# Kernel tuning notes

Measured on AMD Instinct MI355X. Metric: run time of the kernel, lower is better.

## Reference

```python
import jax, jax.numpy as jnp
import numpy as np

WS = 7      # window size
SHIFT = 3   # shift size
NH = 6      # num heads


def _window_partition(x, ws):
    # (b, h, w, c) -> (b * nh_w * nw_w, ws*ws, c)
    b, h, w, c = x.shape
    x = x.reshape(b, h // ws, ws, w // ws, ws, c).transpose(0, 1, 3, 2, 4, 5)
    return x.reshape(-1, ws * ws, c)


def _window_reverse(windows, h, w, ws):
    # (b*nw, ws, ws, c) -> (b, h, w, c)
    b = windows.shape[0] // ((h // ws) * (w // ws))
    x = windows.reshape(b, h // ws, w // ws, ws, ws, -1).transpose(0, 1, 3, 2, 4, 5)
    return x.reshape(b, h, w, -1)


def _rel_pos_index(ws):
    # WindowMSA._double_step_seq + flip, computed statically with numpy
    seq1 = np.arange(ws) * (2 * ws - 1)
    seq2 = np.arange(ws)
    coords = (seq1[:, None] + seq2[None, :]).reshape(-1)  # (ws*ws,)
    rel = coords[:, None] + coords[None, :]
    return np.ascontiguousarray(rel[:, ::-1])  # flip along dim 1


def _shift_mask(h_pad, w_pad, ws, shift):
    # Swin shifted-window attention mask, static numpy computation
    img = np.zeros((h_pad, w_pad), dtype=np.float32)
    slices = (slice(0, -ws), slice(-ws, -shift), slice(-shift, None))
    cnt = 0
    for hs in slices:
        for wsl in slices:
            img[hs, wsl] = cnt
            cnt += 1
    mw = img.reshape(h_pad // ws, ws, w_pad // ws, ws).transpose(0, 2, 1, 3)
    mw = mw.reshape(-1, ws * ws)  # (nw, n)
    diff = mw[:, None, :] - mw[:, :, None]
    return np.where(diff != 0, -100.0, 0.0).astype(np.float32)  # (nw, n, n)


def setup_inputs() -> dict:
    key = jax.random.key(0)
    ks = jax.random.split(key, 5)
    c, b, h, w = 192, 32, 56, 56
    return {
        "query": jax.random.normal(ks[0], (b, h * w, c), jnp.float32),
        "rpb_table": jax.random.normal(ks[1], ((2 * WS - 1) ** 2, NH), jnp.float32) * 0.02,
        "qkv_w": jax.random.normal(ks[2], (3 * c, c), jnp.float32) * 0.02,
        "qkv_b": jnp.zeros((3 * c,), jnp.float32),
        "proj_w": jax.random.normal(ks[3], (c, c), jnp.float32) * 0.02,
        "proj_b": jnp.zeros((c,), jnp.float32),
        "h": h,
        "w": w,
    }


def reference(query, rpb_table, qkv_w, qkv_b, proj_w, proj_b, h, w):
    b, l, c = query.shape
    hd = c // NH
    scale = hd ** (-0.5)
    x = query.reshape(b, h, w, c)
    pad_r = (WS - w % WS) % WS
    pad_b = (WS - h % WS) % WS
    if pad_r > 0 or pad_b > 0:
        x = jnp.pad(x, ((0, 0), (0, pad_b), (0, pad_r), (0, 0)))
    h_pad, w_pad = h + pad_b, w + pad_r

    # cyclic shift + mask
    x = jnp.roll(x, shift=(-SHIFT, -SHIFT), axis=(1, 2))
    attn_mask = jnp.asarray(_shift_mask(h_pad, w_pad, WS, SHIFT))  # (nw, n, n)

    xw = _window_partition(x, WS)  # (b*nw, n, c)
    B_, n, _ = xw.shape
    nw = attn_mask.shape[0]

    # qkv projection
    qkv = (xw @ qkv_w.T + qkv_b).reshape(B_, n, 3, NH, hd).transpose(2, 0, 3, 1, 4)
    q, k, v = qkv[0], qkv[1], qkv[2]  # each (B_, NH, n, hd)

    attn = jnp.einsum('bhqd,bhkd->bhqk', q * scale, k)

    # relative position bias
    rel_idx = jnp.asarray(_rel_pos_index(WS).reshape(-1))
    bias = rpb_table[rel_idx].reshape(n, n, NH).transpose(2, 0, 1)  # (NH, n, n)
    attn = attn + bias[None]

    # shifted-window mask
    attn = attn.reshape(B_ // nw, nw, NH, n, n) + attn_mask[None, :, None]
    attn = attn.reshape(B_, NH, n, n)

    attn = jax.nn.softmax(attn, axis=-1)
    out = jnp.einsum('bhqk,bhkd->bhqd', attn, v).transpose(0, 2, 1, 3).reshape(B_, n, c)
    out = out @ proj_w.T + proj_b

    out = out.reshape(-1, WS, WS, c)
    xr = _window_reverse(out, h_pad, w_pad, WS)
    xr = jnp.roll(xr, shift=(SHIFT, SHIFT), axis=(1, 2))
    if pad_r > 0 or pad_b > 0:
        xr = xr[:, :h, :w, :]
    return xr.reshape(b, h * w, c)
```

## Files before the change

kernel.cpp:

```cpp
#include <hip/hip_runtime.h>

typedef unsigned short u16;
typedef unsigned int   u32;
typedef __bf16 bf16x8 __attribute__((ext_vector_type(8)));
typedef float  f32x4  __attribute__((ext_vector_type(4)));


__device__ __forceinline__ u16 f2b(float f){
  return __builtin_bit_cast(u16, (__bf16)f);
}
__device__ __forceinline__ u32 pk2(float a, float b){
  return (u32)f2b(a) | ((u32)f2b(b) << 16);
}

__device__ __forceinline__ int coords_fn(int t){ return (t/7)*13 + (t%7); }
__device__ __forceinline__ int code_fn(int t, int wy, int wx){
  const int ty = t/7, tx = t%7;
  const int hp = wy*7 + ty, wp = wx*7 + tx;
  const int rh = (hp < 49) ? 0 : ((hp < 53) ? 1 : 2);
  const int rw = (wp < 49) ? 0 : ((wp < 53) ? 1 : 2);
  return rh*3 + rw;
}

__global__ __launch_bounds__(256) void prep_kernel(const float* __restrict__ qkvw,
                                                   const float* __restrict__ projw,
                                                   const float* __restrict__ rpb,
                                                   u16* __restrict__ wq, u16* __restrict__ wp,
                                                   float* __restrict__ biasC){
  const int i = blockIdx.x * 256 + threadIdx.x;
  if (i < 576*192) wq[i] = f2b(qkvw[i]);
  if (i < 192*192) wp[i] = f2b(projw[i]);
  {
    const int cls = i / 27648, rem = i % 27648;
    const int h = rem / 4608, rem2 = rem % 4608;
    const int ii = rem2 / 72, j = rem2 % 72;
    const int wyR = (cls & 2) ? 7 : 0, wxR = (cls & 1) ? 7 : 0;
    float v = -1e30f;
    if (j < 49){
      const int icl = (ii > 48) ? 48 : ii;
      v = rpb[(coords_fn(icl) + coords_fn(48 - j))*6 + h];
      if (code_fn(icl, wyR, wxR) != code_fn(j, wyR, wxR)) v -= 100.0f;
    }
    biasC[i] = v;
  }
}

__global__ __launch_bounds__(256, 2) void qkv_kernel(const float* __restrict__ x,
    const u16* __restrict__ wq, const float* __restrict__ qb,
    u16* __restrict__ qG, u16* __restrict__ kG, u16* __restrict__ vG)
{
  __shared__ u16 XA[128][200];
  const int wi0 = blockIdx.x * 2;
  const int bb = wi0 >> 6, wy = (wi0 >> 3) & 7;
  const int tid = threadIdx.x;
  const int wave = tid >> 6, lane = tid & 63;
  const int g = lane >> 4, r = lane & 15;
  const f32x4 z4 = {0.f, 0.f, 0.f, 0.f};

  #pragma unroll
  for (int half = 0; half < 2; ++half){
    float4 gv[6][2];
    int grow[6], gc8[6];
    #pragma unroll
    for (int i2 = 0; i2 < 6; ++i2){
      const int idx = half*1536 + i2*256 + tid;
      const int row = idx / 24, c8 = (idx % 24) * 8;
      grow[i2] = row; gc8[i2] = c8;
      const int rl = row & 63;
      const int wx = (wi0 + (row >> 6)) & 7;
      if (rl < 49){
        const int ty = rl / 7, tx = rl % 7;
        int sh = wy*7 + ty + 3; if (sh >= 56) sh -= 56;
        int sw = wx*7 + tx + 3; if (sw >= 56) sw -= 56;
        const float* src = x + (size_t)(((bb*56 + sh)*56 + sw))*192 + c8;
        gv[i2][0] = *reinterpret_cast<const float4*>(src);
        gv[i2][1] = *reinterpret_cast<const float4*>(src + 4);
      } else {
        gv[i2][0] = make_float4(0.f,0.f,0.f,0.f);
        gv[i2][1] = make_float4(0.f,0.f,0.f,0.f);
      }
    }
    #pragma unroll
    for (int i2 = 0; i2 < 6; ++i2){
      uint4 w;
      w.x = pk2(gv[i2][0].x, gv[i2][0].y);
      w.y = pk2(gv[i2][0].z, gv[i2][0].w);
      w.z = pk2(gv[i2][1].x, gv[i2][1].y);
      w.w = pk2(gv[i2][1].z, gv[i2][1].w);
      *reinterpret_cast<uint4*>(&XA[grow[i2]][gc8[i2]]) = w;
    }
  }
  __syncthreads();

  {
    f32x4 acc[8][3];
    #pragma unroll
    for (int mt = 0; mt < 8; ++mt)
      #pragma unroll
      for (int c = 0; c < 3; ++c) acc[mt][c] = z4;
    #pragma unroll
    for (int ks = 0; ks < 6; ++ks){
      bf16x8 aw[3];
      #pragma unroll
      for (int c = 0; c < 3; ++c)
        aw[c] = *reinterpret_cast<const bf16x8*>(wq + (size_t)(wave*48 + c*16 + r)*192 + ks*32 + 8*g);
      bf16x8 ax[8];
      #pragma unroll
      for (int mt = 0; mt < 8; ++mt)
        ax[mt] = *reinterpret_cast<const bf16x8*>(&XA[mt*16 + r][ks*32 + 8*g]);
      #pragma unroll
      for (int mt = 0; mt < 8; ++mt)
        #pragma unroll
        for (int c = 0; c < 3; ++c)
          acc[mt][c] = __builtin_amdgcn_mfma_f32_16x16x32_bf16(aw[c], ax[mt], acc[mt][c], 0, 0, 0);
    }
    const float S = 0.17677669529663687f;
    #pragma unroll
    for (int c = 0; c < 3; ++c){
      const int ch0 = wave*48 + c*16 + 4*g;
      const float4 bi = *reinterpret_cast<const float4*>(qb + ch0);
      #pragma unroll
      for (int mt = 0; mt < 8; ++mt){
        const int u = (wi0 + (mt >> 2))*6 + (ch0 >> 5);
        const int tok = (mt & 3)*16 + r;
        uint2 t;
        t.x = pk2((acc[mt][c][0] + bi.x)*S, (acc[mt][c][1] + bi.y)*S);
        t.y = pk2((acc[mt][c][2] + bi.z)*S, (acc[mt][c][3] + bi.w)*S);
        *reinterpret_cast<uint2*>(qG + ((size_t)u*64 + tok)*32 + (ch0 & 31)) = t;
      }
    }
  }

  {
    f32x4 acc[8][3];
    #pragma unroll
    for (int mt = 0; mt < 8; ++mt)
      #pragma unroll
      for (int c = 0; c < 3; ++c) acc[mt][c] = z4;
    #pragma unroll
    for (int ks = 0; ks < 6; ++ks){
      bf16x8 aw[3];
      #pragma unroll
      for (int c = 0; c < 3; ++c)
        aw[c] = *reinterpret_cast<const bf16x8*>(wq + (size_t)(192 + wave*48 + c*16 + r)*192 + ks*32 + 8*g);
      bf16x8 ax[8];
      #pragma unroll
      for (int mt = 0; mt < 8; ++mt)
        ax[mt] = *reinterpret_cast<const bf16x8*>(&XA[mt*16 + r][ks*32 + 8*g]);
      #pragma unroll
      for (int mt = 0; mt < 8; ++mt)
        #pragma unroll
        for (int c = 0; c < 3; ++c)
          acc[mt][c] = __builtin_amdgcn_mfma_f32_16x16x32_bf16(aw[c], ax[mt], acc[mt][c], 0, 0, 0);
    }
    #pragma unroll
    for (int c = 0; c < 3; ++c){
      const int ch0 = wave*48 + c*16 + 4*g;
      const float4 bi = *reinterpret_cast<const float4*>(qb + 192 + ch0);
      #pragma unroll
      for (int mt = 0; mt < 8; ++mt){
        const int u = (wi0 + (mt >> 2))*6 + (ch0 >> 5);
        const int tok = (mt & 3)*16 + r;
        uint2 t;
        t.x = pk2(acc[mt][c][0] + bi.x, acc[mt][c][1] + bi.y);
        t.y = pk2(acc[mt][c][2] + bi.z, acc[mt][c][3] + bi.w);
        *reinterpret_cast<uint2*>(kG + ((size_t)u*64 + tok)*32 + (ch0 & 31)) = t;
      }
    }
  }

  {
    f32x4 acc[8][3];
    #pragma unroll
    for (int mt = 0; mt < 8; ++mt)
      #pragma unroll
      for (int c = 0; c < 3; ++c) acc[mt][c] = z4;
    #pragma unroll
    for (int ks = 0; ks < 6; ++ks){
      bf16x8 bw[3];
      #pragma unroll
      for (int c = 0; c < 3; ++c)
        bw[c] = *reinterpret_cast<const bf16x8*>(wq + (size_t)(384 + wave*48 + c*16 + r)*192 + ks*32 + 8*g);
      bf16x8 ax[8];
      #pragma unroll
      for (int mt = 0; mt < 8; ++mt)
        ax[mt] = *reinterpret_cast<const bf16x8*>(&XA[mt*16 + r][ks*32 + 8*g]);
      #pragma unroll
      for (int mt = 0; mt < 8; ++mt)
        #pragma unroll
        for (int c = 0; c < 3; ++c)
          acc[mt][c] = __builtin_amdgcn_mfma_f32_16x16x32_bf16(ax[mt], bw[c], acc[mt][c], 0, 0, 0);
    }
    #pragma unroll
    for (int c = 0; c < 3; ++c){
      const int ch = wave*48 + c*16 + r;
      const float bv = qb[384 + ch];
      #pragma unroll
      for (int mt = 0; mt < 8; ++mt){
        const int u = (wi0 + (mt >> 2))*6 + (ch >> 5);
        const int d = ch & 31;
        uint2 t;
        t.x = pk2(acc[mt][c][0] + bv, acc[mt][c][1] + bv);
        t.y = pk2(acc[mt][c][2] + bv, acc[mt][c][3] + bv);
        *reinterpret_cast<uint2*>(vG + ((size_t)u*32 + d)*64 + (mt & 3)*16 + 4*g) = t;
      }
    }
  }
}

__global__ __launch_bounds__(384, 4) void attnproj_kernel(const u16* __restrict__ qG,
    const u16* __restrict__ kG, const u16* __restrict__ vG,
    const float* __restrict__ biasC, const u16* __restrict__ wp,
    const float* __restrict__ pb, float* __restrict__ out)
{
  __shared__ u16 AO[64][200];
  __shared__ u16 Psh[6][2][16][72];
  const int wi = blockIdx.x;
  const int bb = wi >> 6, wy = (wi >> 3) & 7, wx = wi & 7;
  const int tid = threadIdx.x;
  const int h = tid / 64;
  const int lane = tid & 63;
  const int g = lane >> 4, r = lane & 15;
  const int unit = wi*6 + h;
  const int cls = ((wy == 7) ? 2 : 0) + ((wx == 7) ? 1 : 0);
  const float* bC = biasC + ((size_t)(cls*6 + h)*64)*72;
  const u16* qp = qG + (size_t)unit*2048;
  const f32x4 z4 = {0.f, 0.f, 0.f, 0.f};

  bf16x8 ak[4];
  #pragma unroll
  for (int mt = 0; mt < 4; ++mt)
    ak[mt] = *reinterpret_cast<const bf16x8*>(kG + ((size_t)unit*64 + mt*16 + r)*32 + 8*g);
  bf16x8 av[2][2];
  #pragma unroll
  for (int nt = 0; nt < 2; ++nt)
    #pragma unroll
    for (int k2 = 0; k2 < 2; ++k2)
      av[nt][k2] = *reinterpret_cast<const bf16x8*>(vG + ((size_t)unit*32 + nt*16 + r)*64 + k2*32 + 8*g);

  #pragma unroll 2
  for (int mt2 = 0; mt2 < 4; ++mt2){
    const int i_r = mt2*16 + r;
    const bf16x8 aq = *reinterpret_cast<const bf16x8*>(qp + (size_t)i_r*32 + 8*g);
    float4 bf[4];
    #pragma unroll
    for (int mt = 0; mt < 4; ++mt)
      bf[mt] = *reinterpret_cast<const float4*>(bC + (size_t)i_r*72 + mt*16 + 4*g);
    f32x4 s[4];
    #pragma unroll
    for (int mt = 0; mt < 4; ++mt)
      s[mt] = __builtin_amdgcn_mfma_f32_16x16x32_bf16(ak[mt], aq, z4, 0, 0, 0);
    float mx = -1e30f;
    #pragma unroll
    for (int mt = 0; mt < 4; ++mt)
      #pragma unroll
      for (int jj = 0; jj < 4; ++jj){
        const float t = s[mt][jj] + bf[mt][jj];
        s[mt][jj] = t;
        mx = fmaxf(mx, t);
      }
    mx = fmaxf(mx, __shfl_xor(mx, 16));
    mx = fmaxf(mx, __shfl_xor(mx, 32));
    float sum = 0.f;
    #pragma unroll
    for (int mt = 0; mt < 4; ++mt)
      #pragma unroll
      for (int jj = 0; jj < 4; ++jj){
        const float p = __expf(s[mt][jj] - mx);
        s[mt][jj] = p;
        sum += p;
      }
    sum += __shfl_xor(sum, 16);
    sum += __shfl_xor(sum, 32);
    const float rs = 1.0f / sum;
    #pragma unroll
    for (int mt = 0; mt < 4; ++mt){
      uint2 pw;
      pw.x = pk2(s[mt][0]*rs, s[mt][1]*rs);
      pw.y = pk2(s[mt][2]*rs, s[mt][3]*rs);
      *reinterpret_cast<uint2*>(&Psh[h][mt2 & 1][r][16*mt + 4*g]) = pw;
    }
    f32x4 o[2] = {z4, z4};
    #pragma unroll
    for (int k2 = 0; k2 < 2; ++k2){
      const bf16x8 bp = *reinterpret_cast<const bf16x8*>(&Psh[h][mt2 & 1][r][32*k2 + 8*g]);
      #pragma unroll
      for (int nt = 0; nt < 2; ++nt)
        o[nt] = __builtin_amdgcn_mfma_f32_16x16x32_bf16(av[nt][k2], bp, o[nt], 0, 0, 0);
    }
    #pragma unroll
    for (int nt = 0; nt < 2; ++nt){
      uint2 t;
      t.x = pk2(o[nt][0], o[nt][1]);
      t.y = pk2(o[nt][2], o[nt][3]);
      *reinterpret_cast<uint2*>(&AO[i_r][h*32 + nt*16 + 4*g]) = t;
    }
  }
  __syncthreads();

  {
    f32x4 pacc[4][2];
    #pragma unroll
    for (int mt = 0; mt < 4; ++mt){ pacc[mt][0] = z4; pacc[mt][1] = z4; }
    #pragma unroll
    for (int ks = 0; ks < 6; ++ks){
      bf16x8 a2[4];
      #pragma unroll
      for (int mt = 0; mt < 4; ++mt)
        a2[mt] = *reinterpret_cast<const bf16x8*>(&AO[mt*16 + r][ks*32 + 8*g]);
      #pragma unroll
      for (int nt = 0; nt < 2; ++nt){
        const bf16x8 bw = *reinterpret_cast<const bf16x8*>(wp + (size_t)(h*32 + nt*16 + r)*192 + ks*32 + 8*g);
        #pragma unroll
        for (int mt = 0; mt < 4; ++mt)
          pacc[mt][nt] = __builtin_amdgcn_mfma_f32_16x16x32_bf16(a2[mt], bw, pacc[mt][nt], 0, 0, 0);
      }
    }
    #pragma unroll
    for (int nt = 0; nt < 2; ++nt){
      const int n = h*32 + nt*16 + r;
      const float bias = pb[n];
      #pragma unroll
      for (int mt = 0; mt < 4; ++mt)
        #pragma unroll
        for (int jj = 0; jj < 4; ++jj){
          const int tok = mt*16 + 4*g + jj;
          if (tok < 49){
            const int ty = tok/7, tx = tok%7;
            int dh = wy*7 + ty + 3; if (dh >= 56) dh -= 56;
            int dw = wx*7 + tx + 3; if (dw >= 56) dw -= 56;
            out[(size_t)((bb*56 + dh)*56 + dw)*192 + n] = pacc[mt][nt][jj] + bias;
          }
        }
    }
  }
}

extern "C" void kernel_launch(void* const* d_in, const int* in_sizes, int n_in,
                              void* d_out, int out_size, void* d_ws, size_t ws_size,
                              hipStream_t stream) {
  const float* x     = (const float*)d_in[0];
  const float* rpb   = (const float*)d_in[1];
  const float* qkvw  = (const float*)d_in[2];
  const float* qkvb  = (const float*)d_in[3];
  const float* projw = (const float*)d_in[4];
  const float* projb = (const float*)d_in[5];
  float* out = (float*)d_out;

  char* ws = (char*)d_ws;
  u16*   wq    = (u16*)(ws);
  u16*   wpj   = (u16*)(ws + 221184);
  float* biasC = (float*)(ws + 221184 + 73728);
  u16*   qG    = (u16*)(ws + 737280);
  u16*   kG    = (u16*)(ws + 737280 + 1ll*50331648);
  u16*   vG    = (u16*)(ws + 737280 + 2ll*50331648);

  prep_kernel    <<<432, 256, 0, stream>>>(qkvw, projw, rpb, wq, wpj, biasC);
  qkv_kernel     <<<1024, 256, 0, stream>>>(x, wq, qkvb, qG, kG, vG);
  attnproj_kernel<<<2048, 384, 0, stream>>>(qG, kG, vG, biasC, wpj, projb, out);
}
```

Baseline: 138.7 us.

## Retile Q/K/V and proj weight buffers into fragment-friendly layouts

```diff
diff --git a/kernel.cpp b/kernel.cpp
--- a/kernel.cpp
+++ b/kernel.cpp
@@ -11,6 +11,10 @@
 }
 __device__ __forceinline__ u32 pk2(float a, float b){
   return (u32)f2b(a) | ((u32)f2b(b) << 16);
+}
+__device__ __forceinline__ bf16x8 pack8(uint2 a, uint2 b){
+  uint4 t; t.x = a.x; t.y = a.y; t.z = b.x; t.w = b.y;
+  return __builtin_bit_cast(bf16x8, t);
 }
 
 __device__ __forceinline__ int coords_fn(int t){ return (t/7)*13 + (t%7); }
@@ -25,11 +29,22 @@
 __global__ __launch_bounds__(256) void prep_kernel(const float* __restrict__ qkvw,
                                                    const float* __restrict__ projw,
                                                    const float* __restrict__ rpb,
-                                                   u16* __restrict__ wq, u16* __restrict__ wp,
+                                                   u16* __restrict__ wq, u16* __restrict__ wpF,
                                                    float* __restrict__ biasC){
   const int i = blockIdx.x * 256 + threadIdx.x;
   if (i < 576*192) wq[i] = f2b(qkvw[i]);
-  if (i < 192*192) wp[i] = f2b(projw[i]);
+  if (i < 4608){
+    const int f = i >> 6, l = i & 63;
+    const int rt = f / 6, ks = f % 6;
+    const int g = l >> 4, r = l & 15;
+    const float* src = projw + (size_t)(rt*16 + r)*192 + ks*32 + 8*g;
+    const float4 a = *reinterpret_cast<const float4*>(src);
+    const float4 b = *reinterpret_cast<const float4*>(src + 4);
+    uint4 w;
+    w.x = pk2(a.x, a.y); w.y = pk2(a.z, a.w);
+    w.z = pk2(b.x, b.y); w.w = pk2(b.z, b.w);
+    *reinterpret_cast<uint4*>(wpF + (size_t)i*8) = w;
+  }
   {
     const int cls = i / 27648, rem = i % 27648;
     const int h = rem / 4608, rem2 = rem % 4608;
@@ -119,6 +134,7 @@
     for (int c = 0; c < 3; ++c){
       const int ch0 = wave*48 + c*16 + 4*g;
       const float4 bi = *reinterpret_cast<const float4*>(qb + ch0);
+      const int chq = (ch0 & 31) >> 2;
       #pragma unroll
       for (int mt = 0; mt < 8; ++mt){
         const int u = (wi0 + (mt >> 2))*6 + (ch0 >> 5);
@@ -126,7 +142,7 @@
         uint2 t;
         t.x = pk2((acc[mt][c][0] + bi.x)*S, (acc[mt][c][1] + bi.y)*S);
         t.y = pk2((acc[mt][c][2] + bi.z)*S, (acc[mt][c][3] + bi.w)*S);
-        *reinterpret_cast<uint2*>(qG + ((size_t)u*64 + tok)*32 + (ch0 & 31)) = t;
+        *reinterpret_cast<uint2*>(qG + (((size_t)u*8 + chq)*64 + tok)*4) = t;
       }
     }
   }
@@ -157,6 +173,7 @@
     for (int c = 0; c < 3; ++c){
       const int ch0 = wave*48 + c*16 + 4*g;
       const float4 bi = *reinterpret_cast<const float4*>(qb + 192 + ch0);
+      const int chq = (ch0 & 31) >> 2;
       #pragma unroll
       for (int mt = 0; mt < 8; ++mt){
         const int u = (wi0 + (mt >> 2))*6 + (ch0 >> 5);
@@ -164,7 +181,7 @@
         uint2 t;
         t.x = pk2(acc[mt][c][0] + bi.x, acc[mt][c][1] + bi.y);
         t.y = pk2(acc[mt][c][2] + bi.z, acc[mt][c][3] + bi.w);
-        *reinterpret_cast<uint2*>(kG + ((size_t)u*64 + tok)*32 + (ch0 & 31)) = t;
+        *reinterpret_cast<uint2*>(kG + (((size_t)u*8 + chq)*64 + tok)*4) = t;
       }
     }
   }
@@ -195,14 +212,15 @@
     for (int c = 0; c < 3; ++c){
       const int ch = wave*48 + c*16 + r;
       const float bv = qb[384 + ch];
+      const int d = ch & 31;
       #pragma unroll
       for (int mt = 0; mt < 8; ++mt){
         const int u = (wi0 + (mt >> 2))*6 + (ch >> 5);
-        const int d = ch & 31;
+        const int tokq = (mt & 3)*4 + g;
         uint2 t;
         t.x = pk2(acc[mt][c][0] + bv, acc[mt][c][1] + bv);
         t.y = pk2(acc[mt][c][2] + bv, acc[mt][c][3] + bv);
-        *reinterpret_cast<uint2*>(vG + ((size_t)u*32 + d)*64 + (mt & 3)*16 + 4*g) = t;
+        *reinterpret_cast<uint2*>(vG + (((size_t)u*16 + tokq)*32 + d)*4) = t;
       }
     }
   }
@@ -210,7 +228,7 @@
 
 __global__ __launch_bounds__(384, 4) void attnproj_kernel(const u16* __restrict__ qG,
     const u16* __restrict__ kG, const u16* __restrict__ vG,
-    const float* __restrict__ biasC, const u16* __restrict__ wp,
+    const float* __restrict__ biasC, const u16* __restrict__ wpF,
     const float* __restrict__ pb, float* __restrict__ out)
 {
   __shared__ u16 AO[64][200];
@@ -224,24 +242,31 @@
   const int unit = wi*6 + h;
   const int cls = ((wy == 7) ? 2 : 0) + ((wx == 7) ? 1 : 0);
   const float* bC = biasC + ((size_t)(cls*6 + h)*64)*72;
-  const u16* qp = qG + (size_t)unit*2048;
   const f32x4 z4 = {0.f, 0.f, 0.f, 0.f};
 
   bf16x8 ak[4];
   #pragma unroll
-  for (int mt = 0; mt < 4; ++mt)
-    ak[mt] = *reinterpret_cast<const bf16x8*>(kG + ((size_t)unit*64 + mt*16 + r)*32 + 8*g);
+  for (int mt = 0; mt < 4; ++mt){
+    const uint2 a = *reinterpret_cast<const uint2*>(kG + (((size_t)unit*8 + 2*g    )*64 + mt*16 + r)*4);
+    const uint2 b = *reinterpret_cast<const uint2*>(kG + (((size_t)unit*8 + 2*g + 1)*64 + mt*16 + r)*4);
+    ak[mt] = pack8(a, b);
+  }
   bf16x8 av[2][2];
   #pragma unroll
   for (int nt = 0; nt < 2; ++nt)
     #pragma unroll
-    for (int k2 = 0; k2 < 2; ++k2)
-      av[nt][k2] = *reinterpret_cast<const bf16x8*>(vG + ((size_t)unit*32 + nt*16 + r)*64 + k2*32 + 8*g);
+    for (int k2 = 0; k2 < 2; ++k2){
+      const uint2 a = *reinterpret_cast<const uint2*>(vG + (((size_t)unit*16 + k2*8 + 2*g    )*32 + nt*16 + r)*4);
+      const uint2 b = *reinterpret_cast<const uint2*>(vG + (((size_t)unit*16 + k2*8 + 2*g + 1)*32 + nt*16 + r)*4);
+      av[nt][k2] = pack8(a, b);
+    }
 
   #pragma unroll 2
   for (int mt2 = 0; mt2 < 4; ++mt2){
     const int i_r = mt2*16 + r;
-    const bf16x8 aq = *reinterpret_cast<const bf16x8*>(qp + (size_t)i_r*32 + 8*g);
+    const uint2 qa = *reinterpret_cast<const uint2*>(qG + (((size_t)unit*8 + 2*g    )*64 + i_r)*4);
+    const uint2 qb2 = *reinterpret_cast<const uint2*>(qG + (((size_t)unit*8 + 2*g + 1)*64 + i_r)*4);
+    const bf16x8 aq = pack8(qa, qb2);
     float4 bf[4];
     #pragma unroll
     for (int mt = 0; mt < 4; ++mt)
@@ -310,7 +335,7 @@
         a2[mt] = *reinterpret_cast<const bf16x8*>(&AO[mt*16 + r][ks*32 + 8*g]);
       #pragma unroll
       for (int nt = 0; nt < 2; ++nt){
-        const bf16x8 bw = *reinterpret_cast<const bf16x8*>(wp + (size_t)(h*32 + nt*16 + r)*192 + ks*32 + 8*g);
+        const bf16x8 bw = *reinterpret_cast<const bf16x8*>(wpF + (((size_t)(h*2 + nt)*6 + ks)*64 + lane)*8);
         #pragma unroll
         for (int mt = 0; mt < 4; ++mt)
           pacc[mt][nt] = __builtin_amdgcn_mfma_f32_16x16x32_bf16(a2[mt], bw, pacc[mt][nt], 0, 0, 0);
@@ -349,13 +374,13 @@
 
   char* ws = (char*)d_ws;
   u16*   wq    = (u16*)(ws);
-  u16*   wpj   = (u16*)(ws + 221184);
+  u16*   wpF   = (u16*)(ws + 221184);
   float* biasC = (float*)(ws + 221184 + 73728);
   u16*   qG    = (u16*)(ws + 737280);
   u16*   kG    = (u16*)(ws + 737280 + 1ll*50331648);
   u16*   vG    = (u16*)(ws + 737280 + 2ll*50331648);
 
-  prep_kernel    <<<432, 256, 0, stream>>>(qkvw, projw, rpb, wq, wpj, biasC);
+  prep_kernel    <<<432, 256, 0, stream>>>(qkvw, projw, rpb, wq, wpF, biasC);
   qkv_kernel     <<<1024, 256, 0, stream>>>(x, wq, qkvb, qG, kG, vG);
-  attnproj_kernel<<<2048, 384, 0, stream>>>(qG, kG, vG, biasC, wpj, projb, out);
-}
+  attnproj_kernel<<<2048, 384, 0, stream>>>(qG, kG, vG, biasC, wpF, projb, out);
+}
```

After: 122.3 us. -11.8%, faster.
